# Performance work log

Hardware: AMD Instinct MI355X
Metric: run time of the kernel (lower is better)

The kernel has to match this reference:

```python
import jax, jax.numpy as jnp
import numpy as np

B, K, N, D, H, NNEG, NTOP = 8, 8, 128, 256, 128, 64, 64
UNARY_SCALES = (1.0, 1.0, 1.0)  # one scale per tree level, tree_height = log2(K) = 3


def setup_inputs():
    key = jax.random.key(0)
    ks = jax.random.split(key, 8)
    s = 0.05
    return {
        'pos_fea': jax.random.normal(ks[0], (B, K, N, D), jnp.float32),
        'neg_fea': jax.random.normal(ks[1], (B * K, NNEG, D), jnp.float32),
        'pos_classes': jax.random.randint(ks[2], (B, K, N), 0, 20),
        'target_class': jax.random.randint(ks[3], (B,), 0, 20),
        'Wp1': jax.random.normal(ks[4], (2 * D, H), jnp.float32) * s,
        'bp1': jnp.zeros((H,), jnp.float32),
        'Wp2': jax.random.normal(ks[5], (H, 1), jnp.float32) * s,
        'bp2': jnp.zeros((1,), jnp.float32),
        'Wu1': jax.random.normal(ks[6], (2 * D, H), jnp.float32) * s,
        'bu1': jnp.zeros((H,), jnp.float32),
        'Wu2': jax.random.normal(ks[7], (H, 1), jnp.float32) * s,
        'bu2': jnp.zeros((1,), jnp.float32),
    }


def _relation(f0, f1, W1, b1, W2, b2):
    # RelationModule: Dense(H, relu) -> Dense(1) applied to concat([f0_m, f1_n])
    # for every cross pair; concat-Dense is split into two GEMMs. -> [Bn, M0, M1]
    d = f0.shape[-1]
    h0 = jnp.einsum('bmd,dh->bmh', f0, W1[:d])
    h1 = jnp.einsum('bnd,dh->bnh', f1, W1[d:])
    h = jax.nn.relu(h0[:, :, None, :] + h1[:, None, :, :] + b1)
    return jnp.einsum('bmnh,h->bmn', h, W2[:, 0]) + b2[0]


def _bg(t, idx):
    # batched_gather along axis 1: t [Bn, P, ...], idx [Bn, T]
    ie = idx.reshape(idx.shape + (1,) * (t.ndim - 2))
    ie = jnp.broadcast_to(ie, idx.shape + t.shape[2:])
    return jnp.take_along_axis(t, ie, axis=1)


def _rep(fea, sub):
    # subproblem representative feature: fea [Bn,S,N,D], sub [Bn,M,S] -> [Bn,M,D]
    idx = jnp.swapaxes(sub, 1, 2)[..., None]              # [Bn,S,M,1]
    idx = jnp.broadcast_to(idx, idx.shape[:-1] + (fea.shape[-1],))
    return jnp.take_along_axis(fea, idx, axis=2).mean(axis=1)


def _tree(pos_fea, neg_fea, Wp1, bp1, Wp2, bp2, Wu1, bu1, Wu2, bu2):
    pos_flat = pos_fea.reshape(B * K, N, D)
    # UnaryModule: mean relation score of each positive proposal vs the negative bag
    ue = _relation(pos_flat, neg_fea, Wu1, bu1, Wu2, bu2).mean(-1)   # [B*K, N]
    sub = jnp.broadcast_to(jnp.arange(N, dtype=jnp.int32)[None, :, None], (B * K, N, 1))
    pe = jnp.zeros_like(ue)
    tree_height = int(np.log2(K))
    best = None
    for i in range(tree_height):
        S = 2 ** i                      # subproblem size per branch at this level
        Bn = sub.shape[0] // 2
        M = sub.shape[1]
        sub2 = sub.reshape(Bn, 2, M, S)  # [::2] / [1::2] split of adjacent rows
        sub0, sub1 = sub2[:, 0], sub2[:, 1]
        pe2 = pe.reshape(Bn, 2, M)
        ue2 = ue.reshape(Bn, 2, M)
        fea = pos_flat.reshape(Bn, 2, S, N, D)
        rep0 = _rep(fea[:, 0], sub0)
        rep1 = _rep(fea[:, 1], sub1)
        # PairwiseCrossSimilarity: scores for all cross pairs of candidates
        scores = _relation(rep0, rep1, Wp1, bp1, Wp2, bp2).reshape(Bn, M * M)
        p0 = jnp.repeat(jnp.arange(M), M)
        p1 = jnp.tile(jnp.arange(M), M)
        pe = pe2[:, 0][:, p0] + pe2[:, 1][:, p1] - scores
        ue = ue2[:, 0][:, p0] + ue2[:, 1][:, p1]
        total = pe + UNARY_SCALES[i] * ue
        sub = jnp.concatenate([sub0[:, p0], sub1[:, p1]], axis=-1)  # [Bn, M*M, 2S]
        topk = 1 if i == tree_height - 1 else min(M * M, NTOP)
        _, inds = jax.lax.top_k(-total, topk)
        sub = _bg(sub, inds)
        ue = jnp.take_along_axis(ue, inds, axis=1)
        pe = jnp.take_along_axis(pe, inds, axis=1)
        best = jnp.take_along_axis(total, inds, axis=1)
    return sub, best


def reference(pos_fea, neg_fea, pos_classes, target_class,
              Wp1, bp1, Wp2, bp2, Wu1, bu1, Wu2, bu2):
    sub, _ = _tree(pos_fea, neg_fea, Wp1, bp1, Wp2, bp2, Wu1, bu1, Wu2, bu2)
    is_target = (pos_classes == target_class[:, None, None]).astype(jnp.float32)
    return sub[:, 0], is_target  # selected proposal per image [B,K], [B,K,N]
```

## Files before the change

kernel.cpp:

```cpp
#include <hip/hip_runtime.h>
#include <stdint.h>

#define B_ 8
#define K_ 8
#define N_ 128
#define D_ 256
#define H_ 128
#define NNEG_ 64

typedef unsigned long long u64;

__device__ __forceinline__ u64 shfl_xor_u64(u64 v, int m) {
    int lo = __shfl_xor((int)(unsigned)v, m, 64);
    int hi = __shfl_xor((int)(unsigned)(v >> 32), m, 64);
    return ((u64)(unsigned)hi << 32) | (unsigned)lo;
}
__device__ __forceinline__ u64 bitonic_merge64(u64 m, int lane) {
#pragma unroll
    for (int j = 32; j > 0; j >>= 1) {
        u64 o = shfl_xor_u64(m, j);
        bool keepMin = ((lane & j) == 0);
        bool lt = m < o;
        m = (keepMin == lt) ? m : o;
    }
    return m;
}
__device__ __forceinline__ u64 merge2(u64 a, u64 b, int lane) {
    u64 br = shfl_xor_u64(b, 63);
    u64 m = a < br ? a : br;
    return bitonic_merge64(m, lane);
}
__device__ __forceinline__ unsigned sortable(float f) {
    unsigned u = __float_as_uint(f);
    return (u & 0x80000000u) ? ~u : (u | 0x80000000u);
}
__device__ __forceinline__ float unsortable(unsigned u) {
    return __uint_as_float((u & 0x80000000u) ? (u & 0x7FFFFFFFu) : ~u);
}
__device__ __forceinline__ void sort128_reg(u64& v0, u64& v1, int lane) {
#pragma unroll
    for (int k = 2; k <= 64; k <<= 1) {
        bool d0 = ((lane & k) == 0);
        bool d1 = (k == 64) ? false : d0;
#pragma unroll
        for (int j = k >> 1; j > 0; j >>= 1) {
            u64 o0 = shfl_xor_u64(v0, j);
            bool km0 = (((lane & j) == 0) == d0);
            v0 = (km0 == (v0 < o0)) ? v0 : o0;
            u64 o1 = shfl_xor_u64(v1, j);
            bool km1 = (((lane & j) == 0) == d1);
            v1 = (km1 == (v1 < o1)) ? v1 : o1;
        }
    }
    if (v0 > v1) { u64 tmp = v0; v0 = v1; v1 = tmp; }
#pragma unroll
    for (int j = 32; j > 0; j >>= 1) {
        bool km = ((lane & j) == 0);
        u64 o0 = shfl_xor_u64(v0, j);
        v0 = (km == (v0 < o0)) ? v0 : o0;
        u64 o1 = shfl_xor_u64(v1, j);
        v1 = (km == (v1 < o1)) ? v1 : o1;
    }
}

__global__ __launch_bounds__(256) void g1_gemm(
    const float* __restrict__ pos, const float* __restrict__ neg,
    const float* __restrict__ Wu1, const float* __restrict__ Wp1,
    const int* __restrict__ pos_classes, const int* __restrict__ target_class,
    float* __restrict__ HU0, float* __restrict__ HU1n,
    float* __restrict__ HP0, float* __restrict__ HP1,
    float* __restrict__ outp) {
    int bid = blockIdx.x;
    int t = threadIdx.x;
    if (bid >= 448) {
        int base = (bid - 448) * 2048 + t * 8;
#pragma unroll
        for (int q = 0; q < 8; ++q) {
            int idx = base + q;
            outp[64 + idx] = (pos_classes[idx] == target_class[idx >> 10]) ? 1.0f : 0.0f;
        }
        return;
    }
    const float* A; const float* W; float* OUT; int rb;
    if (bid < 128)      { A = pos; W = Wu1;           OUT = HU0;  rb = bid * 64; }
    else if (bid < 192) { A = neg; W = Wu1 + D_ * H_; OUT = HU1n; rb = (bid - 128) * 64; }
    else if (bid < 320) { A = pos; W = Wp1;           OUT = HP0;  rb = (bid - 192) * 64; }
    else                { A = pos; W = Wp1 + D_ * H_; OUT = HP1;  rb = (bid - 320) * 64; }

    __shared__ float As[64][17];
    __shared__ float Bs[16][128];
    int tx = t & 15, ty = t >> 4;
    float acc[4][8];
#pragma unroll
    for (int i = 0; i < 4; ++i)
#pragma unroll
        for (int j = 0; j < 8; ++j) acc[i][j] = 0.f;

    for (int k0 = 0; k0 < D_; k0 += 16) {
        {
            int row = t >> 2, kq = (t & 3) * 4;
            const float4 av = *(const float4*)&A[(size_t)(rb + row) * D_ + k0 + kq];
            As[row][kq + 0] = av.x; As[row][kq + 1] = av.y;
            As[row][kq + 2] = av.z; As[row][kq + 3] = av.w;
        }
        {
            int flat = t * 8;
            int kr = flat >> 7, hc = flat & 127;
            float4 b0 = *(const float4*)&W[(size_t)(k0 + kr) * H_ + hc];
            float4 b1 = *(const float4*)&W[(size_t)(k0 + kr) * H_ + hc + 4];
            *(float4*)&Bs[kr][hc] = b0;
            *(float4*)&Bs[kr][hc + 4] = b1;
        }
        __syncthreads();
#pragma unroll
        for (int kk = 0; kk < 16; ++kk) {
            float a0 = As[ty * 4 + 0][kk], a1 = As[ty * 4 + 1][kk];
            float a2 = As[ty * 4 + 2][kk], a3 = As[ty * 4 + 3][kk];
            float bv[8];
            *(float4*)&bv[0] = *(const float4*)&Bs[kk][tx * 8];
            *(float4*)&bv[4] = *(const float4*)&Bs[kk][tx * 8 + 4];
#pragma unroll
            for (int j = 0; j < 8; ++j) {
                acc[0][j] += a0 * bv[j];
                acc[1][j] += a1 * bv[j];
                acc[2][j] += a2 * bv[j];
                acc[3][j] += a3 * bv[j];
            }
        }
        __syncthreads();
    }
#pragma unroll
    for (int i = 0; i < 4; ++i) {
        float4 o0 = {acc[i][0], acc[i][1], acc[i][2], acc[i][3]};
        float4 o1 = {acc[i][4], acc[i][5], acc[i][6], acc[i][7]};
        *(float4*)&OUT[(size_t)(rb + ty * 4 + i) * H_ + tx * 8] = o0;
        *(float4*)&OUT[(size_t)(rb + ty * 4 + i) * H_ + tx * 8 + 4] = o1;
    }
}

__global__ __launch_bounds__(256) void g2_ue_sc0(
    const float* __restrict__ HU0, const float* __restrict__ HU1n,
    const float* __restrict__ bu1, const float* __restrict__ Wu2,
    const float* __restrict__ bu2v,
    const float* __restrict__ HP0, const float* __restrict__ HP1,
    const float* __restrict__ bp1, const float* __restrict__ Wp2,
    const float* __restrict__ bp2,
    float* __restrict__ t0, float* __restrict__ sc0) {
    __shared__ float smem[13568];
    float (*Ls)[129] = (float(*)[129])smem;
    float (*Rs)[129] = (float(*)[129])(smem + 4128);
    float* wsv = smem + 4128 + 8256;
    float (*red)[33] = (float(*)[33])(smem + 4128 + 8256 + 128);

    int bid = blockIdx.x;
    int t = threadIdx.x;
    bool is_ue = bid < 256;

    if (is_ue) {
        int bk = bid >> 2, mt = bid & 3;
        for (int i = t; i < 64 * 128; i += 256) {
            int n = i >> 7, h = i & 127;
            Rs[n][h] = HU1n[(size_t)(bk * NNEG_ + n) * H_ + h];
        }
        for (int i = t; i < 32 * 128; i += 256) {
            int m = i >> 7, h = i & 127;
            Ls[m][h] = HU0[(size_t)(bk * N_ + mt * 32 + m) * H_ + h] + bu1[h];
        }
        if (t < 128) wsv[t] = Wu2[t];
    } else {
        int bid2 = bid - 256;
        int b = bid2 >> 3, m0t = (bid2 >> 1) & 3, m1t = bid2 & 1;
        const float* Lg = HP0 + (size_t)b * 2 * N_ * H_ + m0t * 32 * H_;
        const float* Rg = HP1 + (size_t)b * 2 * N_ * H_ + N_ * H_ + m1t * 64 * H_;
        for (int i = t; i < 64 * 128; i += 256) {
            int n = i >> 7, h = i & 127;
            Rs[n][h] = Rg[(size_t)n * H_ + h];
        }
        for (int i = t; i < 32 * 128; i += 256) {
            int m = i >> 7, h = i & 127;
            Ls[m][h] = Lg[(size_t)m * H_ + h] + bp1[h];
        }
        if (t < 128) wsv[t] = Wp2[t];
    }
    __syncthreads();

    int tm = t & 7, tn = t >> 3;
    const float* l0 = &Ls[tm * 4 + 0][0];
    const float* l1 = &Ls[tm * 4 + 1][0];
    const float* l2 = &Ls[tm * 4 + 2][0];
    const float* l3 = &Ls[tm * 4 + 3][0];
    const float* r0 = &Rs[tn * 2 + 0][0];
    const float* r1 = &Rs[tn * 2 + 1][0];
    float a00 = 0.f, a01 = 0.f, a10 = 0.f, a11 = 0.f;
    float a20 = 0.f, a21 = 0.f, a30 = 0.f, a31 = 0.f;
#pragma unroll 4
    for (int h = 0; h < 128; ++h) {
        float w = wsv[h];
        float b0 = r0[h], b1 = r1[h];
        float a0 = l0[h], a1 = l1[h], a2 = l2[h], a3 = l3[h];
        float v;
        v = a0 + b0; v = v > 0.f ? v : 0.f; a00 += v * w;
        v = a0 + b1; v = v > 0.f ? v : 0.f; a01 += v * w;
        v = a1 + b0; v = v > 0.f ? v : 0.f; a10 += v * w;
        v = a1 + b1; v = v > 0.f ? v : 0.f; a11 += v * w;
        v = a2 + b0; v = v > 0.f ? v : 0.f; a20 += v * w;
        v = a2 + b1; v = v > 0.f ? v : 0.f; a21 += v * w;
        v = a3 + b0; v = v > 0.f ? v : 0.f; a30 += v * w;
        v = a3 + b1; v = v > 0.f ? v : 0.f; a31 += v * w;
    }

    if (is_ue) {
        int bk = bid >> 2, mt = bid & 3;
        red[tm * 4 + 0][tn] = a00 + a01;
        red[tm * 4 + 1][tn] = a10 + a11;
        red[tm * 4 + 2][tn] = a20 + a21;
        red[tm * 4 + 3][tn] = a30 + a31;
        __syncthreads();
        if (t < 32) {
            float s = 0.f;
            for (int q = 0; q < 32; ++q) s += red[t][q];
            t0[bk * N_ + mt * 32 + t] = s * (1.0f / NNEG_) + bu2v[0];
        }
    } else {
        int bid2 = bid - 256;
        int b = bid2 >> 3, m0t = (bid2 >> 1) & 3, m1t = bid2 & 1;
        float bp2v = bp2[0];
        float* orow = sc0 + (size_t)b * 16384;
        float accs[4][2] = {{a00, a01}, {a10, a11}, {a20, a21}, {a30, a31}};
#pragma unroll
        for (int i = 0; i < 4; ++i) {
            int m0 = m0t * 32 + tm * 4 + i;
#pragma unroll
            for (int j = 0; j < 2; ++j) {
                int m1 = m1t * 64 + tn * 2 + j;
                orow[m0 * 128 + m1] = accs[i][j] + bp2v;
            }
        }
    }
}

__global__ __launch_bounds__(256) void g3a_top0(const float* __restrict__ sc0,
                                                const float* __restrict__ t0,
                                                u64* __restrict__ g3c) {
    int bid = blockIdx.x;
    int r = bid >> 3, c = bid & 7;
    int t = threadIdx.x, lane = t & 63, w = t >> 6;
    __shared__ float tt[256];
    __shared__ u64 cand[4][128];
    if (t < 256) tt[t] = t0[r * 256 + t];
    __syncthreads();
    const float* row = sc0 + (size_t)r * 16384 + c * 2048 + w * 512;
    unsigned sv[8];
#pragma unroll
    for (int j = 0; j < 8; ++j) {
        int li = j * 64 + lane;
        int idx = c * 2048 + w * 512 + li;
        float v = (tt[idx >> 7] + tt[128 + (idx & 127)]) - row[li];
        sv[j] = sortable(v);
    }
    unsigned T = 0u;
#pragma unroll
    for (int it = 0; it < 16; ++it) {
        int p = 30 - 2 * it;
        unsigned C1 = T | (1u << p), C2 = T | (2u << p), C3 = T | (3u << p);
        unsigned c1 = 0u, c2 = 0u, c3 = 0u;
#pragma unroll
        for (int j = 0; j < 8; ++j) {
            c1 += (unsigned)__popcll(__ballot(sv[j] < C1));
            c2 += (unsigned)__popcll(__ballot(sv[j] < C2));
            c3 += (unsigned)__popcll(__ballot(sv[j] < C3));
        }
        unsigned k = (c3 < 64u) ? 3u : (c2 < 64u) ? 2u : (c1 < 64u) ? 1u : 0u;
        T |= (k << p);
    }
    u64* my = cand[w];
    int base = 0;
#pragma unroll
    for (int j = 0; j < 8; ++j) {
        u64 mask = __ballot(sv[j] <= T);
        if (sv[j] <= T) {
            int pos = base + (int)__popcll(mask & ((1ull << lane) - 1ull));
            if (pos < 128) {
                int idx = c * 2048 + w * 512 + j * 64 + lane;
                my[pos] = ((u64)sv[j] << 32) | (unsigned)idx;
            }
        }
        base += (int)__popcll(mask);
    }
    int cc = base < 128 ? base : 128;
    u64 v0 = (lane < cc) ? my[lane] : ~0ull;
    u64 v1 = (64 + lane < cc) ? my[64 + lane] : ~0ull;
    sort128_reg(v0, v1, lane);
    my[lane] = v0;
    __syncthreads();
    if (w == 0) {
        u64 x0 = cand[0][lane], x1 = cand[1][lane];
        u64 x2 = cand[2][lane], x3 = cand[3][lane];
        u64 y0 = merge2(x0, x1, lane), y1 = merge2(x2, x3, lane);
        g3c[(size_t)bid * 64 + lane] = merge2(y0, y1, lane);
    }
}

__global__ __launch_bounds__(64) void g3b_merge(const u64* __restrict__ g3c,
                                                float* __restrict__ tA,
                                                int* __restrict__ pA) {
    int r = blockIdx.x;
    int lane = threadIdx.x;
    const u64* Lp = g3c + (size_t)r * 512;
    u64 x0 = Lp[lane], x1 = Lp[64 + lane], x2 = Lp[128 + lane], x3 = Lp[192 + lane];
    u64 x4 = Lp[256 + lane], x5 = Lp[320 + lane], x6 = Lp[384 + lane], x7 = Lp[448 + lane];
    u64 y0 = merge2(x0, x1, lane), y1 = merge2(x2, x3, lane);
    u64 y2 = merge2(x4, x5, lane), y3 = merge2(x6, x7, lane);
    u64 z0 = merge2(y0, y1, lane), z1 = merge2(y2, y3, lane);
    u64 f = merge2(z0, z1, lane);
    int idx = (int)(f & 0xFFFFFFFFull);
    tA[r * 64 + lane] = unsortable((unsigned)(f >> 32));
    pA[r * 64 + lane] = ((idx >> 7) << 8) | (idx & 127);
}

__global__ __launch_bounds__(256) void g4a_s1(
    const float* __restrict__ HP0, const float* __restrict__ HP1,
    const float* __restrict__ tA, const int* __restrict__ pA,
    const float* __restrict__ bp1, const float* __restrict__ Wp2,
    const float* __restrict__ bp2, u64* __restrict__ g4top) {
    int bid = blockIdx.x;
    int u = bid >> 3, mq = (bid >> 1) & 3, nh = bid & 1;
    int t = threadIdx.x, lane = t & 63, w = t >> 6;
    __shared__ float LsT[128][17];
    __shared__ float RsT[128][34];
    __shared__ float taL[16], taR[32];
    __shared__ int paL[16], paR[32];
    __shared__ float wsv[128];
    __shared__ u64 cand[4][64];
    if (t < 16) { taL[t] = tA[(2 * u) * 64 + mq * 16 + t]; paL[t] = pA[(2 * u) * 64 + mq * 16 + t]; }
    else if (t < 48) { int e = t - 16; taR[e] = tA[(2 * u + 1) * 64 + nh * 32 + e]; paR[e] = pA[(2 * u + 1) * 64 + nh * 32 + e]; }
    if (t >= 128) wsv[t - 128] = Wp2[t - 128];
    float bp2v = bp2[0];
    __syncthreads();
    for (int i = t; i < 16 * 128; i += 256) {
        int m = i >> 7, h = i & 127;
        int pk = paL[m]; int a0 = pk >> 8, a1 = pk & 255;
        float s = HP0[(size_t)(4 * u) * 16384 + a0 * 128 + h]
                + HP0[(size_t)(4 * u + 1) * 16384 + a1 * 128 + h];
        LsT[h][m] = s * 0.5f + bp1[h];
    }
    for (int i = t; i < 32 * 128; i += 256) {
        int n = i >> 7, h = i & 127;
        int pk = paR[n]; int c0 = pk >> 8, c1 = pk & 255;
        float s = HP1[(size_t)(4 * u + 2) * 16384 + c0 * 128 + h]
                + HP1[(size_t)(4 * u + 3) * 16384 + c1 * 128 + h];
        RsT[h][n] = s * 0.5f;
    }
    __syncthreads();
    int lm = w * 4 + (lane >> 4);
    int ln = lane & 15;
    float a0 = 0.f, a1 = 0.f;
#pragma unroll 4
    for (int h = 0; h < 128; ++h) {
        float lv = LsT[h][lm];
        float2 rv = *(const float2*)&RsT[h][ln * 2];
        float wv = wsv[h];
        float v;
        v = lv + rv.x; v = v > 0.f ? v : 0.f; a0 += v * wv;
        v = lv + rv.y; v = v > 0.f ? v : 0.f; a1 += v * wv;
    }
    int m_unit = mq * 16 + lm;
    int n0 = nh * 32 + ln * 2;
    float val0 = (taL[lm] + taR[ln * 2 + 0]) - (a0 + bp2v);
    float val1 = (taL[lm] + taR[ln * 2 + 1]) - (a1 + bp2v);
    u64 v0 = ((u64)sortable(val0) << 32) | (unsigned)(m_unit * 64 + n0);
    u64 v1 = ((u64)sortable(val1) << 32) | (unsigned)(m_unit * 64 + n0 + 1);
    sort128_reg(v0, v1, lane);
    cand[w][lane] = v0;
    __syncthreads();
    if (w == 0) {
        u64 x0 = cand[0][lane], x1 = cand[1][lane];
        u64 x2 = cand[2][lane], x3 = cand[3][lane];
        u64 y0 = merge2(x0, x1, lane), y1 = merge2(x2, x3, lane);
        g4top[(size_t)bid * 64 + lane] = merge2(y0, y1, lane);
    }
}

__global__ __launch_bounds__(256) void g4b_s2(
    const float* __restrict__ HP0, const float* __restrict__ HP1,
    const int* __restrict__ pA, const u64* __restrict__ g4top,
    const float* __restrict__ bp1, const float* __restrict__ Wp2,
    const float* __restrict__ bp2, float* __restrict__ outp) {
    int b = blockIdx.x;
    int t = threadIdx.x, lane = t & 63, w = t >> 6;
    __shared__ float LsT[128][68];
    __shared__ float RsT[128][36];
    __shared__ float tL[64], tR[64];
    __shared__ unsigned subL[64], subR[64];
    __shared__ float wsv[128];
    __shared__ u64 sred[4];
    if (t < 128) wsv[t] = Wp2[t];
    float bp2v = bp2[0];
    if (w < 2) {
        const u64* Lp = g4top + (size_t)(2 * b + w) * 512;
        u64 x0 = Lp[lane], x1 = Lp[64 + lane], x2 = Lp[128 + lane], x3 = Lp[192 + lane];
        u64 x4 = Lp[256 + lane], x5 = Lp[320 + lane], x6 = Lp[384 + lane], x7 = Lp[448 + lane];
        u64 y0 = merge2(x0, x1, lane), y1 = merge2(x2, x3, lane);
        u64 y2 = merge2(x4, x5, lane), y3 = merge2(x6, x7, lane);
        u64 z0 = merge2(y0, y1, lane), z1 = merge2(y2, y3, lane);
        u64 m = merge2(z0, z1, lane);
        int idx = (int)(m & 0xFFFFFFFFull);
        int p0 = idx >> 6, p1 = idx & 63;
        float val = unsortable((unsigned)(m >> 32));
        int rowL = 4 * b + 2 * w;
        int pkL = pA[rowL * 64 + p0];
        int pkR = pA[(rowL + 1) * 64 + p1];
        unsigned leaves = ((unsigned)pkL << 16) | (unsigned)pkR;
        if (w == 0) { tL[lane] = val; subL[lane] = leaves; }
        else        { tR[lane] = val; subR[lane] = leaves; }
    }
    __syncthreads();
    for (int i = t; i < 64 * 128; i += 256) {
        int m = i >> 7, h = i & 127;
        unsigned s4 = subL[m];
        float s = HP0[(size_t)(8 * b + 0) * 16384 + ((s4 >> 24) & 255u) * 128 + h]
                + HP0[(size_t)(8 * b + 1) * 16384 + ((s4 >> 16) & 255u) * 128 + h]
                + HP0[(size_t)(8 * b + 2) * 16384 + ((s4 >> 8) & 255u) * 128 + h]
                + HP0[(size_t)(8 * b + 3) * 16384 + (s4 & 255u) * 128 + h];
        LsT[h][m] = s * 0.25f + bp1[h];
    }
    u64 best = ~0ull;
    int qm = w * 4 + (lane >> 4);
    int qn = lane & 15;
    for (int half = 0; half < 2; ++half) {
        __syncthreads();
        for (int i = t; i < 32 * 128; i += 256) {
            int n = i >> 7, h = i & 127;
            int ng = half * 32 + n;
            unsigned s4 = subR[ng];
            float s = HP1[(size_t)(8 * b + 4) * 16384 + ((s4 >> 24) & 255u) * 128 + h]
                    + HP1[(size_t)(8 * b + 5) * 16384 + ((s4 >> 16) & 255u) * 128 + h]
                    + HP1[(size_t)(8 * b + 6) * 16384 + ((s4 >> 8) & 255u) * 128 + h]
                    + HP1[(size_t)(8 * b + 7) * 16384 + (s4 & 255u) * 128 + h];
            RsT[h][n] = s * 0.25f;
        }
        __syncthreads();
        float acc[4][2];
#pragma unroll
        for (int i = 0; i < 4; ++i) { acc[i][0] = 0.f; acc[i][1] = 0.f; }
#pragma unroll 2
        for (int h = 0; h < 128; ++h) {
            float4 lv = *(const float4*)&LsT[h][qm * 4];
            float2 rv = *(const float2*)&RsT[h][qn * 2];
            float wv = wsv[h];
            float v;
            v = lv.x + rv.x; v = v > 0.f ? v : 0.f; acc[0][0] += v * wv;
            v = lv.x + rv.y; v = v > 0.f ? v : 0.f; acc[0][1] += v * wv;
            v = lv.y + rv.x; v = v > 0.f ? v : 0.f; acc[1][0] += v * wv;
            v = lv.y + rv.y; v = v > 0.f ? v : 0.f; acc[1][1] += v * wv;
            v = lv.z + rv.x; v = v > 0.f ? v : 0.f; acc[2][0] += v * wv;
            v = lv.z + rv.y; v = v > 0.f ? v : 0.f; acc[2][1] += v * wv;
            v = lv.w + rv.x; v = v > 0.f ? v : 0.f; acc[3][0] += v * wv;
            v = lv.w + rv.y; v = v > 0.f ? v : 0.f; acc[3][1] += v * wv;
        }
#pragma unroll
        for (int mi = 0; mi < 4; ++mi) {
#pragma unroll
            for (int nj = 0; nj < 2; ++nj) {
                int m = qm * 4 + mi;
                int ng = half * 32 + qn * 2 + nj;
                float val = (tL[m] + tR[ng]) - (acc[mi][nj] + bp2v);
                u64 kk = ((u64)sortable(val) << 32) | (unsigned)(m * 64 + ng);
                best = kk < best ? kk : best;
            }
        }
    }
#pragma unroll
    for (int off = 32; off > 0; off >>= 1) {
        u64 o = shfl_xor_u64(best, off);
        best = o < best ? o : best;
    }
    if (lane == 0) sred[w] = best;
    __syncthreads();
    if (t == 0) {
        u64 bb = sred[0];
        for (int p = 1; p < 4; ++p) { u64 o = sred[p]; bb = o < bb ? o : bb; }
        int idx = (int)(bb & 0xFFFFFFFFull);
        unsigned sl = subL[idx >> 6], sr = subR[idx & 63];
        outp[b * 8 + 0] = (float)((sl >> 24) & 255u);
        outp[b * 8 + 1] = (float)((sl >> 16) & 255u);
        outp[b * 8 + 2] = (float)((sl >> 8) & 255u);
        outp[b * 8 + 3] = (float)(sl & 255u);
        outp[b * 8 + 4] = (float)((sr >> 24) & 255u);
        outp[b * 8 + 5] = (float)((sr >> 16) & 255u);
        outp[b * 8 + 6] = (float)((sr >> 8) & 255u);
        outp[b * 8 + 7] = (float)(sr & 255u);
    }
}

extern "C" void kernel_launch(void* const* d_in, const int* in_sizes, int n_in,
                              void* d_out, int out_size, void* d_ws, size_t ws_size,
                              hipStream_t stream) {
    const float* pos = (const float*)d_in[0];
    const float* neg = (const float*)d_in[1];
    const int* pos_classes = (const int*)d_in[2];
    const int* target_class = (const int*)d_in[3];
    const float* Wp1 = (const float*)d_in[4];
    const float* bp1 = (const float*)d_in[5];
    const float* Wp2 = (const float*)d_in[6];
    const float* bp2 = (const float*)d_in[7];
    const float* Wu1 = (const float*)d_in[8];
    const float* bu1 = (const float*)d_in[9];
    const float* Wu2 = (const float*)d_in[10];
    const float* bu2 = (const float*)d_in[11];

    float* wsf = (float*)d_ws;
    float* HU0 = wsf;
    float* HP0 = HU0 + 1048576;
    float* HP1 = HP0 + 1048576;
    float* HU1n = HP1 + 1048576;
    float* t0 = HU1n + 524288;
    float* sc0 = t0 + 8192;
    float* tA = sc0 + 524288;
    int* pA = (int*)(tA + 2048);
    u64* g3c = (u64*)wsf;
    u64* g4top = (u64*)wsf + 16384;
    float* outp = (float*)d_out;

    g1_gemm<<<452, 256, 0, stream>>>(pos, neg, Wu1, Wp1, pos_classes,
                                     target_class, HU0, HU1n, HP0, HP1, outp);
    g2_ue_sc0<<<512, 256, 0, stream>>>(HU0, HU1n, bu1, Wu2, bu2,
                                       HP0, HP1, bp1, Wp2, bp2, t0, sc0);
    g3a_top0<<<256, 256, 0, stream>>>(sc0, t0, g3c);
    g3b_merge<<<32, 64, 0, stream>>>(g3c, tA, pA);
    g4a_s1<<<128, 256, 0, stream>>>(HP0, HP1, tA, pA, bp1, Wp2, bp2, g4top);
    g4b_s2<<<8, 256, 0, stream>>>(HP0, HP1, pA, g4top, bp1, Wp2, bp2, outp);
}
```

Before: 180.3 us.

## Transpose shared tiles in GEMM and relation kernels, fuse merge into stage-1

The projection GEMM now stages A transposed in shared memory with a 32-deep k tile, so each thread reads its four A values as one float4. The relation kernel stores L and R transposed so the inner loop does vector LDS reads instead of strided scalar ones. The separate g3b merge kernel is removed and its bitonic merge is recomputed inside each g4a block, which drops one launch but repeats the merge work redundantly across blocks.

```diff
diff --git a/kernel.cpp b/kernel.cpp
--- a/kernel.cpp
+++ b/kernel.cpp
@@ -87,8 +87,8 @@
     else if (bid < 320) { A = pos; W = Wp1;           OUT = HP0;  rb = (bid - 192) * 64; }
     else                { A = pos; W = Wp1 + D_ * H_; OUT = HP1;  rb = (bid - 320) * 64; }
 
-    __shared__ float As[64][17];
-    __shared__ float Bs[16][128];
+    __shared__ float AsT[32][68];
+    __shared__ float Bs[32][128];
     int tx = t & 15, ty = t >> 4;
     float acc[4][8];
 #pragma unroll
@@ -96,29 +96,31 @@
 #pragma unroll
         for (int j = 0; j < 8; ++j) acc[i][j] = 0.f;
 
-    for (int k0 = 0; k0 < D_; k0 += 16) {
-        {
-            int row = t >> 2, kq = (t & 3) * 4;
-            const float4 av = *(const float4*)&A[(size_t)(rb + row) * D_ + k0 + kq];
-            As[row][kq + 0] = av.x; As[row][kq + 1] = av.y;
-            As[row][kq + 2] = av.z; As[row][kq + 3] = av.w;
-        }
-        {
-            int flat = t * 8;
-            int kr = flat >> 7, hc = flat & 127;
-            float4 b0 = *(const float4*)&W[(size_t)(k0 + kr) * H_ + hc];
-            float4 b1 = *(const float4*)&W[(size_t)(k0 + kr) * H_ + hc + 4];
-            *(float4*)&Bs[kr][hc] = b0;
-            *(float4*)&Bs[kr][hc + 4] = b1;
+    for (int k0 = 0; k0 < D_; k0 += 32) {
+#pragma unroll
+        for (int rep = 0; rep < 2; ++rep) {
+            int flat = t + rep * 256;
+            int row = flat >> 3, kq = flat & 7;
+            const float4 av = *(const float4*)&A[(size_t)(rb + row) * D_ + k0 + kq * 4];
+            AsT[kq * 4 + 0][row] = av.x;
+            AsT[kq * 4 + 1][row] = av.y;
+            AsT[kq * 4 + 2][row] = av.z;
+            AsT[kq * 4 + 3][row] = av.w;
+        }
+#pragma unroll
+        for (int rep = 0; rep < 4; ++rep) {
+            int i = t + rep * 256;
+            int kr = i >> 5, hcq = i & 31;
+            *(float4*)&Bs[kr][hcq * 4] = *(const float4*)&W[(size_t)(k0 + kr) * H_ + hcq * 4];
         }
         __syncthreads();
-#pragma unroll
-        for (int kk = 0; kk < 16; ++kk) {
-            float a0 = As[ty * 4 + 0][kk], a1 = As[ty * 4 + 1][kk];
-            float a2 = As[ty * 4 + 2][kk], a3 = As[ty * 4 + 3][kk];
+#pragma unroll 8
+        for (int kk = 0; kk < 32; ++kk) {
+            const float4 av = *(const float4*)&AsT[kk][ty * 4];
             float bv[8];
             *(float4*)&bv[0] = *(const float4*)&Bs[kk][tx * 8];
             *(float4*)&bv[4] = *(const float4*)&Bs[kk][tx * 8 + 4];
+            float a0 = av.x, a1 = av.y, a2 = av.z, a3 = av.w;
 #pragma unroll
             for (int j = 0; j < 8; ++j) {
                 acc[0][j] += a0 * bv[j];
@@ -146,67 +148,65 @@
     const float* __restrict__ bp1, const float* __restrict__ Wp2,
     const float* __restrict__ bp2,
     float* __restrict__ t0, float* __restrict__ sc0) {
-    __shared__ float smem[13568];
-    float (*Ls)[129] = (float(*)[129])smem;
-    float (*Rs)[129] = (float(*)[129])(smem + 4128);
-    float* wsv = smem + 4128 + 8256;
-    float (*red)[33] = (float(*)[33])(smem + 4128 + 8256 + 128);
+    __shared__ float LsT[128][36];
+    __shared__ float RsT[128][66];
+    __shared__ float wsv[128];
+    __shared__ float red[32][33];
 
     int bid = blockIdx.x;
     int t = threadIdx.x;
     bool is_ue = bid < 256;
 
+    const float* Lsrc; const float* Rsrc; const float* b1v; const float* W2;
     if (is_ue) {
         int bk = bid >> 2, mt = bid & 3;
-        for (int i = t; i < 64 * 128; i += 256) {
-            int n = i >> 7, h = i & 127;
-            Rs[n][h] = HU1n[(size_t)(bk * NNEG_ + n) * H_ + h];
-        }
-        for (int i = t; i < 32 * 128; i += 256) {
-            int m = i >> 7, h = i & 127;
-            Ls[m][h] = HU0[(size_t)(bk * N_ + mt * 32 + m) * H_ + h] + bu1[h];
-        }
-        if (t < 128) wsv[t] = Wu2[t];
+        Lsrc = HU0 + (size_t)(bk * N_ + mt * 32) * H_;
+        Rsrc = HU1n + (size_t)bk * NNEG_ * H_;
+        b1v = bu1; W2 = Wu2;
     } else {
         int bid2 = bid - 256;
         int b = bid2 >> 3, m0t = (bid2 >> 1) & 3, m1t = bid2 & 1;
-        const float* Lg = HP0 + (size_t)b * 2 * N_ * H_ + m0t * 32 * H_;
-        const float* Rg = HP1 + (size_t)b * 2 * N_ * H_ + N_ * H_ + m1t * 64 * H_;
-        for (int i = t; i < 64 * 128; i += 256) {
-            int n = i >> 7, h = i & 127;
-            Rs[n][h] = Rg[(size_t)n * H_ + h];
-        }
-        for (int i = t; i < 32 * 128; i += 256) {
-            int m = i >> 7, h = i & 127;
-            Ls[m][h] = Lg[(size_t)m * H_ + h] + bp1[h];
-        }
-        if (t < 128) wsv[t] = Wp2[t];
-    }
+        Lsrc = HP0 + (size_t)b * 2 * N_ * H_ + m0t * 32 * H_;
+        Rsrc = HP1 + (size_t)b * 2 * N_ * H_ + N_ * H_ + m1t * 64 * H_;
+        b1v = bp1; W2 = Wp2;
+    }
+    for (int i = t; i < 32 * 32; i += 256) {
+        int m = i & 31, hq = i >> 5;
+        const float4 a = *(const float4*)&Lsrc[(size_t)m * H_ + hq * 4];
+        const float4 b = *(const float4*)&b1v[hq * 4];
+        LsT[hq * 4 + 0][m] = a.x + b.x;
+        LsT[hq * 4 + 1][m] = a.y + b.y;
+        LsT[hq * 4 + 2][m] = a.z + b.z;
+        LsT[hq * 4 + 3][m] = a.w + b.w;
+    }
+    for (int i = t; i < 64 * 32; i += 256) {
+        int n = i & 63, hq = i >> 6;
+        const float4 a = *(const float4*)&Rsrc[(size_t)n * H_ + hq * 4];
+        RsT[hq * 4 + 0][n] = a.x;
+        RsT[hq * 4 + 1][n] = a.y;
+        RsT[hq * 4 + 2][n] = a.z;
+        RsT[hq * 4 + 3][n] = a.w;
+    }
+    if (t < 128) wsv[t] = W2[t];
     __syncthreads();
 
     int tm = t & 7, tn = t >> 3;
-    const float* l0 = &Ls[tm * 4 + 0][0];
-    const float* l1 = &Ls[tm * 4 + 1][0];
-    const float* l2 = &Ls[tm * 4 + 2][0];
-    const float* l3 = &Ls[tm * 4 + 3][0];
-    const float* r0 = &Rs[tn * 2 + 0][0];
-    const float* r1 = &Rs[tn * 2 + 1][0];
     float a00 = 0.f, a01 = 0.f, a10 = 0.f, a11 = 0.f;
     float a20 = 0.f, a21 = 0.f, a30 = 0.f, a31 = 0.f;
 #pragma unroll 4
     for (int h = 0; h < 128; ++h) {
+        const float4 lv = *(const float4*)&LsT[h][tm * 4];
+        const float2 rv = *(const float2*)&RsT[h][tn * 2];
         float w = wsv[h];
-        float b0 = r0[h], b1 = r1[h];
-        float a0 = l0[h], a1 = l1[h], a2 = l2[h], a3 = l3[h];
         float v;
-        v = a0 + b0; v = v > 0.f ? v : 0.f; a00 += v * w;
-        v = a0 + b1; v = v > 0.f ? v : 0.f; a01 += v * w;
-        v = a1 + b0; v = v > 0.f ? v : 0.f; a10 += v * w;
-        v = a1 + b1; v = v > 0.f ? v : 0.f; a11 += v * w;
-        v = a2 + b0; v = v > 0.f ? v : 0.f; a20 += v * w;
-        v = a2 + b1; v = v > 0.f ? v : 0.f; a21 += v * w;
-        v = a3 + b0; v = v > 0.f ? v : 0.f; a30 += v * w;
-        v = a3 + b1; v = v > 0.f ? v : 0.f; a31 += v * w;
+        v = lv.x + rv.x; v = v > 0.f ? v : 0.f; a00 += v * w;
+        v = lv.x + rv.y; v = v > 0.f ? v : 0.f; a01 += v * w;
+        v = lv.y + rv.x; v = v > 0.f ? v : 0.f; a10 += v * w;
+        v = lv.y + rv.y; v = v > 0.f ? v : 0.f; a11 += v * w;
+        v = lv.z + rv.x; v = v > 0.f ? v : 0.f; a20 += v * w;
+        v = lv.z + rv.y; v = v > 0.f ? v : 0.f; a21 += v * w;
+        v = lv.w + rv.x; v = v > 0.f ? v : 0.f; a30 += v * w;
+        v = lv.w + rv.y; v = v > 0.f ? v : 0.f; a31 += v * w;
     }
 
     if (is_ue) {
@@ -301,26 +301,9 @@
     }
 }
 
-__global__ __launch_bounds__(64) void g3b_merge(const u64* __restrict__ g3c,
-                                                float* __restrict__ tA,
-                                                int* __restrict__ pA) {
-    int r = blockIdx.x;
-    int lane = threadIdx.x;
-    const u64* Lp = g3c + (size_t)r * 512;
-    u64 x0 = Lp[lane], x1 = Lp[64 + lane], x2 = Lp[128 + lane], x3 = Lp[192 + lane];
-    u64 x4 = Lp[256 + lane], x5 = Lp[320 + lane], x6 = Lp[384 + lane], x7 = Lp[448 + lane];
-    u64 y0 = merge2(x0, x1, lane), y1 = merge2(x2, x3, lane);
-    u64 y2 = merge2(x4, x5, lane), y3 = merge2(x6, x7, lane);
-    u64 z0 = merge2(y0, y1, lane), z1 = merge2(y2, y3, lane);
-    u64 f = merge2(z0, z1, lane);
-    int idx = (int)(f & 0xFFFFFFFFull);
-    tA[r * 64 + lane] = unsortable((unsigned)(f >> 32));
-    pA[r * 64 + lane] = ((idx >> 7) << 8) | (idx & 127);
-}
-
 __global__ __launch_bounds__(256) void g4a_s1(
     const float* __restrict__ HP0, const float* __restrict__ HP1,
-    const float* __restrict__ tA, const int* __restrict__ pA,
+    const u64* __restrict__ g3c, int* __restrict__ pA,
     const float* __restrict__ bp1, const float* __restrict__ Wp2,
     const float* __restrict__ bp2, u64* __restrict__ g4top) {
     int bid = blockIdx.x;
@@ -328,25 +311,41 @@
     int t = threadIdx.x, lane = t & 63, w = t >> 6;
     __shared__ float LsT[128][17];
     __shared__ float RsT[128][34];
-    __shared__ float taL[16], taR[32];
-    __shared__ int paL[16], paR[32];
+    __shared__ float taL[64], taR[64];
+    __shared__ int paL[64], paR[64];
     __shared__ float wsv[128];
     __shared__ u64 cand[4][64];
-    if (t < 16) { taL[t] = tA[(2 * u) * 64 + mq * 16 + t]; paL[t] = pA[(2 * u) * 64 + mq * 16 + t]; }
-    else if (t < 48) { int e = t - 16; taR[e] = tA[(2 * u + 1) * 64 + nh * 32 + e]; paR[e] = pA[(2 * u + 1) * 64 + nh * 32 + e]; }
+    if (w < 2) {
+        const u64* Lp = g3c + (size_t)(2 * u + w) * 512;
+        u64 x0 = Lp[lane], x1 = Lp[64 + lane], x2 = Lp[128 + lane], x3 = Lp[192 + lane];
+        u64 x4 = Lp[256 + lane], x5 = Lp[320 + lane], x6 = Lp[384 + lane], x7 = Lp[448 + lane];
+        u64 y0 = merge2(x0, x1, lane), y1 = merge2(x2, x3, lane);
+        u64 y2 = merge2(x4, x5, lane), y3 = merge2(x6, x7, lane);
+        u64 z0 = merge2(y0, y1, lane), z1 = merge2(y2, y3, lane);
+        u64 f = merge2(z0, z1, lane);
+        int idx = (int)(f & 0xFFFFFFFFull);
+        int pk = ((idx >> 7) << 8) | (idx & 127);
+        float tv = unsortable((unsigned)(f >> 32));
+        if (w == 0) { taL[lane] = tv; paL[lane] = pk; }
+        else        { taR[lane] = tv; paR[lane] = pk; }
+    }
     if (t >= 128) wsv[t - 128] = Wp2[t - 128];
     float bp2v = bp2[0];
     __syncthreads();
+    if ((bid & 7) == 0) {
+        if (t < 64) pA[(2 * u) * 64 + t] = paL[t];
+        else if (t < 128) pA[(2 * u + 1) * 64 + (t - 64)] = paR[t - 64];
+    }
     for (int i = t; i < 16 * 128; i += 256) {
         int m = i >> 7, h = i & 127;
-        int pk = paL[m]; int a0 = pk >> 8, a1 = pk & 255;
+        int pk = paL[mq * 16 + m]; int a0 = pk >> 8, a1 = pk & 255;
         float s = HP0[(size_t)(4 * u) * 16384 + a0 * 128 + h]
                 + HP0[(size_t)(4 * u + 1) * 16384 + a1 * 128 + h];
         LsT[h][m] = s * 0.5f + bp1[h];
     }
     for (int i = t; i < 32 * 128; i += 256) {
         int n = i >> 7, h = i & 127;
-        int pk = paR[n]; int c0 = pk >> 8, c1 = pk & 255;
+        int pk = paR[nh * 32 + n]; int c0 = pk >> 8, c1 = pk & 255;
         float s = HP1[(size_t)(4 * u + 2) * 16384 + c0 * 128 + h]
                 + HP1[(size_t)(4 * u + 3) * 16384 + c1 * 128 + h];
         RsT[h][n] = s * 0.5f;
@@ -358,7 +357,7 @@
 #pragma unroll 4
     for (int h = 0; h < 128; ++h) {
         float lv = LsT[h][lm];
-        float2 rv = *(const float2*)&RsT[h][ln * 2];
+        const float2 rv = *(const float2*)&RsT[h][ln * 2];
         float wv = wsv[h];
         float v;
         v = lv + rv.x; v = v > 0.f ? v : 0.f; a0 += v * wv;
@@ -366,8 +365,8 @@
     }
     int m_unit = mq * 16 + lm;
     int n0 = nh * 32 + ln * 2;
-    float val0 = (taL[lm] + taR[ln * 2 + 0]) - (a0 + bp2v);
-    float val1 = (taL[lm] + taR[ln * 2 + 1]) - (a1 + bp2v);
+    float val0 = (taL[mq * 16 + lm] + taR[nh * 32 + ln * 2 + 0]) - (a0 + bp2v);
+    float val1 = (taL[mq * 16 + lm] + taR[nh * 32 + ln * 2 + 1]) - (a1 + bp2v);
     u64 v0 = ((u64)sortable(val0) << 32) | (unsigned)(m_unit * 64 + n0);
     u64 v1 = ((u64)sortable(val1) << 32) | (unsigned)(m_unit * 64 + n0 + 1);
     sort128_reg(v0, v1, lane);
@@ -445,8 +444,8 @@
         for (int i = 0; i < 4; ++i) { acc[i][0] = 0.f; acc[i][1] = 0.f; }
 #pragma unroll 2
         for (int h = 0; h < 128; ++h) {
-            float4 lv = *(const float4*)&LsT[h][qm * 4];
-            float2 rv = *(const float2*)&RsT[h][qn * 2];
+            const float4 lv = *(const float4*)&LsT[h][qm * 4];
+            const float2 rv = *(const float2*)&RsT[h][qn * 2];
             float wv = wsv[h];
             float v;
             v = lv.x + rv.x; v = v > 0.f ? v : 0.f; acc[0][0] += v * wv;
@@ -516,8 +515,7 @@
     float* HU1n = HP1 + 1048576;
     float* t0 = HU1n + 524288;
     float* sc0 = t0 + 8192;
-    float* tA = sc0 + 524288;
-    int* pA = (int*)(tA + 2048);
+    int* pA = (int*)(sc0 + 524288);
     u64* g3c = (u64*)wsf;
     u64* g4top = (u64*)wsf + 16384;
     float* outp = (float*)d_out;
@@ -527,7 +525,6 @@
     g2_ue_sc0<<<512, 256, 0, stream>>>(HU0, HU1n, bu1, Wu2, bu2,
                                        HP0, HP1, bp1, Wp2, bp2, t0, sc0);
     g3a_top0<<<256, 256, 0, stream>>>(sc0, t0, g3c);
-    g3b_merge<<<32, 64, 0, stream>>>(g3c, tA, pA);
-    g4a_s1<<<128, 256, 0, stream>>>(HP0, HP1, tA, pA, bp1, Wp2, bp2, g4top);
+    g4a_s1<<<128, 256, 0, stream>>>(HP0, HP1, g3c, pA, bp1, Wp2, bp2, g4top);
     g4b_s2<<<8, 256, 0, stream>>>(HP0, HP1, pA, g4top, bp1, Wp2, bp2, outp);
 }
```

Result: no change. 178.6 us (-1.0%).
